# Performance work log

Measured on AMD Instinct MI355X. Metric: run time of the kernel, lower is better.

The kernel has to match this reference:

```python
import jax, jax.numpy as jnp
import numpy as np

B, N, DIM, HEADS = 8, 1024, 512, 8
HEAD_DIM = DIM // HEADS
SCALE = HEAD_DIM ** -0.5
NEG_BIG = -1.0e12


def setup_inputs() -> dict:
    key = jax.random.key(0)
    k_x, k_qw, k_qb, k_pw, k_pb = jax.random.split(key, 5)
    # torch nn.Linear layout: weight [out, in], y = x @ W.T + b
    s_qkv = (DIM) ** -0.5
    return {
        "x": jax.random.normal(k_x, (B, N, DIM), dtype=jnp.float32),
        "qkv_w": jax.random.uniform(k_qw, (3 * DIM, DIM), minval=-s_qkv, maxval=s_qkv, dtype=jnp.float32),
        "qkv_b": jax.random.uniform(k_qb, (3 * DIM,), minval=-s_qkv, maxval=s_qkv, dtype=jnp.float32),
        "proj_w": jax.random.uniform(k_pw, (DIM, DIM), minval=-s_qkv, maxval=s_qkv, dtype=jnp.float32),
        "proj_b": jax.random.uniform(k_pb, (DIM,), minval=-s_qkv, maxval=s_qkv, dtype=jnp.float32),
    }


def reference(x, qkv_w, qkv_b, proj_w, proj_b):
    b, n, c = x.shape
    qkv = x @ qkv_w.T + qkv_b                      # [B, N, 3*C]
    qkv = qkv.reshape(b, n, 3, HEADS, c // HEADS)
    qkv = jnp.transpose(qkv, (2, 0, 3, 1, 4))      # [3, B, H, N, hd]
    q, k, v = qkv[0], qkv[1], qkv[2]
    attn = jnp.einsum("bhqd,bhkd->bhqk", q, k) * SCALE  # [B, H, N, N]
    # bernoulli(p=0.5) mask added as -1e12 bias (deterministic key)
    mask = jax.random.bernoulli(jax.random.key(42), 0.5, attn.shape)
    attn = attn + mask.astype(attn.dtype) * NEG_BIG
    attn = jax.nn.softmax(attn, axis=-1)
    # dropout p=0.0 -> identity
    out = jnp.einsum("bhqk,bhkd->bhqd", attn, v)   # [B, H, N, hd]
    out = jnp.transpose(out, (0, 2, 1, 3)).reshape(b, n, c)
    return out @ proj_w.T + proj_b
```

## Files before the change

### kernel.cpp

```cpp
#include <hip/hip_runtime.h>
#include <stdint.h>

typedef uint32_t u32;
typedef unsigned long long u64;
using bf16x8 = __attribute__((ext_vector_type(8))) short;
using f32x4  = __attribute__((ext_vector_type(4))) float;

#define MFMA16(a, b, c) __builtin_amdgcn_mfma_f32_16x16x32_bf16((a), (b), (c), 0, 0, 0)

__device__ __forceinline__ unsigned short f2bf(float f) {
  u32 u = __builtin_bit_cast(u32, f);
  return (unsigned short)((u + 0x7FFFu + ((u >> 16) & 1u)) >> 16);
}

__device__ __forceinline__ void gl_lds16(const unsigned short* g, unsigned short* l) {
  __builtin_amdgcn_global_load_lds((const __attribute__((address_space(1))) void*)g,
                                   (__attribute__((address_space(3))) void*)l, 16, 0, 0);
}

__device__ __forceinline__ u32 rotl(u32 x, int r) {
  return __builtin_amdgcn_alignbit(x, x, 32 - r);
}
#define TFR(r) x0 += x1; x1 = rotl(x1, r) ^ x0;

__device__ __forceinline__ u32 tf_word(u32 j) {
  const u32 ks1 = 42u, ks2 = 0x1BD11BDAu ^ 42u;
  u32 x0 = 0u;
  u32 x1 = j + ks1;
  TFR(13) TFR(15) TFR(26) TFR(6)
  x0 += ks1; x1 += ks2 + 1u;
  TFR(17) TFR(29) TFR(16) TFR(24)
  x0 += ks2; x1 += 2u;
  TFR(13) TFR(15) TFR(26) TFR(6)
  x1 += ks1 + 3u;
  TFR(17) TFR(29) TFR(16) TFR(24)
  x0 += ks1; x1 += ks2 + 4u;
  TFR(13) TFR(15) TFR(26) TFR(6)
  x0 += ks2; x1 += 5u;
  return x0 ^ x1;
}

__global__ __launch_bounds__(256) void cvt_kernel(
    const float* __restrict__ x, const float* __restrict__ qw, const float* __restrict__ pw,
    unsigned short* __restrict__ xb, unsigned short* __restrict__ qwb,
    unsigned short* __restrict__ pwb) {
  int t = blockIdx.x * 256 + threadIdx.x;
  const float4* src; unsigned short* dst; int idx;
  if (t < 1048576)      { src = (const float4*)x;  dst = xb;  idx = t; }
  else if (t < 1245184) { src = (const float4*)qw; dst = qwb; idx = t - 1048576; }
  else                  { src = (const float4*)pw; dst = pwb; idx = t - 1245184; }
  float4 v = src[idx];
  ushort4 o = make_ushort4(f2bf(v.x), f2bf(v.y), f2bf(v.z), f2bf(v.w));
  ((ushort4*)dst)[idx] = o;
}

template<int EPI>
__global__ __launch_bounds__(256)
void gemm_kernel(const unsigned short* __restrict__ A, const unsigned short* __restrict__ Bm,
                 const float* __restrict__ bias, unsigned short* __restrict__ q_out,
                 unsigned short* __restrict__ k_out, unsigned short* __restrict__ vt_out,
                 float* __restrict__ f_out) {
  __shared__ __align__(16) unsigned short lA[128 * 32];
  __shared__ __align__(16) unsigned short lB[128 * 32];
  const int tid = threadIdx.x;
  const int lane = tid & 63, w = tid >> 6;
  const int hi = lane >> 4, lo = lane & 15;
  const int wm = w >> 1, wn = w & 1;
  const int m0 = blockIdx.y * 128, n0 = blockIdx.x * 128;
  const int srow = lane >> 2, skc = (lane & 3) * 8;

  f32x4 acc[4][4];
#pragma unroll
  for (int i = 0; i < 4; ++i)
#pragma unroll
    for (int j = 0; j < 4; ++j) acc[i][j] = (f32x4){0.f, 0.f, 0.f, 0.f};

  for (int kt = 0; kt < 16; ++kt) {
    const int k0 = kt * 32;
    __syncthreads();
#pragma unroll
    for (int c = 0; c < 2; ++c) {
      const int rr = (w * 2 + c) * 16 + srow;
      gl_lds16(A  + (size_t)(m0 + rr) * 512 + k0 + skc, &lA[(w * 2 + c) * 512]);
      gl_lds16(Bm + (size_t)(n0 + rr) * 512 + k0 + skc, &lB[(w * 2 + c) * 512]);
    }
    __syncthreads();

    bf16x8 af[4], bfr[4];
#pragma unroll
    for (int i = 0; i < 4; ++i) af[i]  = *(const bf16x8*)&lA[(wm * 64 + i * 16 + lo) * 32 + hi * 8];
#pragma unroll
    for (int i = 0; i < 4; ++i) bfr[i] = *(const bf16x8*)&lB[(wn * 64 + i * 16 + lo) * 32 + hi * 8];
#pragma unroll
    for (int i = 0; i < 4; ++i)
#pragma unroll
      for (int j = 0; j < 4; ++j)
        acc[i][j] = MFMA16(af[i], bfr[j], acc[i][j]);
  }

#pragma unroll
  for (int i = 0; i < 4; ++i) {
    const int rowb = m0 + wm * 64 + i * 16 + hi * 4;
#pragma unroll
    for (int j = 0; j < 4; ++j) {
      const int col = n0 + wn * 64 + j * 16 + lo;
      const float bv = bias[col];
      if (EPI == 0) {
        const int which = col >> 9, hh = (col >> 6) & 7, dd = col & 63;
        const float scl = (which == 0) ? 0.18033688011112042f : 1.0f;
#pragma unroll
        for (int r = 0; r < 4; ++r) {
          const int tok = rowb + r;
          const int b = tok >> 10, nt = tok & 1023;
          const int bh = b * 8 + hh;
          const unsigned short val = f2bf((acc[i][j][r] + bv) * scl);
          if (which == 0)      q_out[((size_t)((bh << 10) + nt)) * 64 + dd] = val;
          else if (which == 1) k_out[((size_t)((bh << 10) + nt)) * 64 + dd] = val;
          else                 vt_out[((size_t)bh * 64 + dd) * 1024 + nt] = val;
        }
      } else {
#pragma unroll
        for (int r = 0; r < 4; ++r)
          f_out[(size_t)(rowb + r) * 512 + col] = acc[i][j][r] + bv;
      }
    }
  }
}

__global__ __launch_bounds__(256, 8) void attn_kernel(
    const unsigned short* __restrict__ Qb, const unsigned short* __restrict__ Kb,
    const unsigned short* __restrict__ VTb, unsigned short* __restrict__ aout) {
  __shared__ __align__(16) unsigned short plds[4][1088];
  const int tid = threadIdx.x;
  const int lane = tid & 63, w = tid >> 6;
  const int hi = lane >> 4, lo = lane & 15;
  const int p = w & 1, half = w >> 1;
  const int bid = blockIdx.x;
  const int xcd = bid & 7, slot = bid >> 3;
  const int bh = (xcd << 3) | (slot >> 5);
  const int qg = slot & 31;
  const int qs = qg * 32 + p * 16;

  bf16x8 qf[2];
#pragma unroll
  for (int dh = 0; dh < 2; ++dh)
    qf[dh] = *(const bf16x8*)&Qb[((size_t)(bh << 10) + qs + lo) * 64 + dh * 32 + hi * 8];

  f32x4 acc[4];
  f32x4 sacc = (f32x4){0.f, 0.f, 0.f, 0.f};
#pragma unroll
  for (int dt = 0; dt < 4; ++dt) acc[dt] = (f32x4){0.f, 0.f, 0.f, 0.f};
  bf16x8 ones;
#pragma unroll
  for (int j = 0; j < 8; ++j) ones[j] = (short)0x3F80;

  const u32 jbase = ((u32)bh << 20) | ((u32)(qs + lo) << 10) | (u32)(hi * 4);
  const int ktbase = half * 8;
  unsigned short* mp = &plds[w][0];

  for (int i = 0; i < 8; ++i) {
    const int k0 = (ktbase + i) * 64;

#pragma unroll
    for (int t = 0; t < 4; ++t) {
      const unsigned short* kbp = &Kb[((size_t)(bh << 10) + k0 + t * 16 + lo) * 64 + hi * 8];
      f32x4 z = (f32x4){0.f, 0.f, 0.f, 0.f};
      z = MFMA16(*(const bf16x8*)kbp, qf[0], z);
      z = MFMA16(*(const bf16x8*)(kbp + 32), qf[1], z);

      float pv[4];
#pragma unroll
      for (int r = 0; r < 4; ++r) {
        const int keepn = (int)tf_word(jbase + (u32)(k0 + t * 16 + r));
        pv[r] = (keepn < 0) ? exp2f(z[r]) : 0.f;
      }
      u32 u0, u1;
      asm("v_cvt_pk_bf16_f32 %0, %1, %2" : "=v"(u0) : "v"(pv[0]), "v"(pv[1]));
      asm("v_cvt_pk_bf16_f32 %0, %1, %2" : "=v"(u1) : "v"(pv[2]), "v"(pv[3]));
      *reinterpret_cast<u64*>(&mp[lo * 68 + t * 16 + hi * 4]) = ((u64)u1 << 32) | (u64)u0;
    }

    bf16x8 pf[2];
#pragma unroll
    for (int ks = 0; ks < 2; ++ks)
      pf[ks] = *(const bf16x8*)&mp[lo * 68 + ks * 32 + hi * 8];
    sacc = MFMA16(pf[0], ones, sacc);
    sacc = MFMA16(pf[1], ones, sacc);
#pragma unroll
    for (int dt = 0; dt < 4; ++dt) {
      const unsigned short* vbp = &VTb[((size_t)(bh * 64 + dt * 16 + lo)) * 1024 + k0 + hi * 8];
      acc[dt] = MFMA16(pf[0], *(const bf16x8*)vbp, acc[dt]);
      acc[dt] = MFMA16(pf[1], *(const bf16x8*)(vbp + 32), acc[dt]);
    }
  }

  float* fb = ((float*)&plds[0][0]) + p * 1040;
  __syncthreads();
  if (half == 1) {
#pragma unroll
    for (int dt = 0; dt < 4; ++dt)
#pragma unroll
      for (int r = 0; r < 4; ++r)
        fb[(hi * 4 + r) * 64 + dt * 16 + lo] = acc[dt][r];
    if (lo == 0)
#pragma unroll
      for (int r = 0; r < 4; ++r) fb[1024 + hi * 4 + r] = sacc[r];
  }
  __syncthreads();
  if (half == 0) {
    const int b = bh >> 3, h = bh & 7;
#pragma unroll
    for (int r = 0; r < 4; ++r) {
      const float zt = sacc[r] + fb[1024 + hi * 4 + r];
      const float inv = 1.0f / zt;
      const int tok = (b << 10) + qs + hi * 4 + r;
#pragma unroll
      for (int dt = 0; dt < 4; ++dt) {
        const float av = acc[dt][r] + fb[(hi * 4 + r) * 64 + dt * 16 + lo];
        aout[(size_t)tok * 512 + h * 64 + dt * 16 + lo] = f2bf(av * inv);
      }
    }
  }
}

extern "C" void kernel_launch(void* const* d_in, const int* in_sizes, int n_in,
                              void* d_out, int out_size, void* d_ws, size_t ws_size,
                              hipStream_t stream) {
  const float* x      = (const float*)d_in[0];
  const float* qkv_w  = (const float*)d_in[1];
  const float* qkv_b  = (const float*)d_in[2];
  const float* proj_w = (const float*)d_in[3];
  const float* proj_b = (const float*)d_in[4];
  float* out = (float*)d_out;
  char* ws = (char*)d_ws;

  unsigned short* xb  = (unsigned short*)(ws);
  unsigned short* qwb = (unsigned short*)(ws +  8388608);
  unsigned short* pwb = (unsigned short*)(ws +  9961472);
  unsigned short* Qb  = (unsigned short*)(ws + 10485760);
  unsigned short* Kb  = (unsigned short*)(ws + 18874368);
  unsigned short* VTb = (unsigned short*)(ws + 27262976);

  cvt_kernel<<<5120, 256, 0, stream>>>(x, qkv_w, proj_w, xb, qwb, pwb);
  gemm_kernel<0><<<dim3(12, 64), 256, 0, stream>>>(xb, qwb, qkv_b, Qb, Kb, VTb, nullptr);
  attn_kernel<<<2048, 256, 0, stream>>>(Qb, Kb, VTb, xb);
  gemm_kernel<1><<<dim3(4, 64), 256, 0, stream>>>(xb, pwb, proj_b, nullptr, nullptr, nullptr, out);
}
```

Before: 205.7 us.

## Fuse fp32-to-bf16 conversion into GEMM loads and simplify mask/exp path

Removes the separate conversion kernel. The GEMMs now read fp32 x and fp32 weights directly, convert them in registers and store bf16 into LDS, in place of the async global-to-LDS loads. The attention mask now uses raw v_exp_f32 with a bitwise AND against the sign of the threefry word, replacing the branch around exp2f. This saves one launch and a write/read round trip of the bf16 copies, but weights are re-converted by every block and the GEMM loses direct-to-LDS loads, so more register traffic goes through the loop.

```diff
diff --git a/kernel.cpp b/kernel.cpp
--- a/kernel.cpp
+++ b/kernel.cpp
@@ -16,6 +16,12 @@
 __device__ __forceinline__ void gl_lds16(const unsigned short* g, unsigned short* l) {
   __builtin_amdgcn_global_load_lds((const __attribute__((address_space(1))) void*)g,
                                    (__attribute__((address_space(3))) void*)l, 16, 0, 0);
+}
+
+__device__ __forceinline__ u32 cvtpk(float a, float b) {
+  u32 r;
+  asm("v_cvt_pk_bf16_f32 %0, %1, %2" : "=v"(r) : "v"(a), "v"(b));
+  return r;
 }
 
 __device__ __forceinline__ u32 rotl(u32 x, int r) {
@@ -40,26 +46,11 @@
   return x0 ^ x1;
 }
 
-__global__ __launch_bounds__(256) void cvt_kernel(
-    const float* __restrict__ x, const float* __restrict__ qw, const float* __restrict__ pw,
-    unsigned short* __restrict__ xb, unsigned short* __restrict__ qwb,
-    unsigned short* __restrict__ pwb) {
-  int t = blockIdx.x * 256 + threadIdx.x;
-  const float4* src; unsigned short* dst; int idx;
-  if (t < 1048576)      { src = (const float4*)x;  dst = xb;  idx = t; }
-  else if (t < 1245184) { src = (const float4*)qw; dst = qwb; idx = t - 1048576; }
-  else                  { src = (const float4*)pw; dst = pwb; idx = t - 1245184; }
-  float4 v = src[idx];
-  ushort4 o = make_ushort4(f2bf(v.x), f2bf(v.y), f2bf(v.z), f2bf(v.w));
-  ((ushort4*)dst)[idx] = o;
-}
-
 template<int EPI>
 __global__ __launch_bounds__(256)
-void gemm_kernel(const unsigned short* __restrict__ A, const unsigned short* __restrict__ Bm,
-                 const float* __restrict__ bias, unsigned short* __restrict__ q_out,
-                 unsigned short* __restrict__ k_out, unsigned short* __restrict__ vt_out,
-                 float* __restrict__ f_out) {
+void gemm_kernel(const void* Ap, const float* B32, const float* __restrict__ bias,
+                 unsigned short* __restrict__ q_out, unsigned short* __restrict__ k_out,
+                 unsigned short* __restrict__ vt_out, float* __restrict__ f_out) {
   __shared__ __align__(16) unsigned short lA[128 * 32];
   __shared__ __align__(16) unsigned short lB[128 * 32];
   const int tid = threadIdx.x;
@@ -81,8 +72,20 @@
 #pragma unroll
     for (int c = 0; c < 2; ++c) {
       const int rr = (w * 2 + c) * 16 + srow;
-      gl_lds16(A  + (size_t)(m0 + rr) * 512 + k0 + skc, &lA[(w * 2 + c) * 512]);
-      gl_lds16(Bm + (size_t)(n0 + rr) * 512 + k0 + skc, &lB[(w * 2 + c) * 512]);
+      const int loff = (w * 2 + c) * 512 + srow * 32 + skc;
+      if (EPI == 0) {
+        const float* ga = (const float*)Ap + (size_t)(m0 + rr) * 512 + k0 + skc;
+        float4 a0 = *(const float4*)ga, a1 = *(const float4*)(ga + 4);
+        uint4 pa = {cvtpk(a0.x, a0.y), cvtpk(a0.z, a0.w), cvtpk(a1.x, a1.y), cvtpk(a1.z, a1.w)};
+        *reinterpret_cast<uint4*>(&lA[loff]) = pa;
+      } else {
+        gl_lds16((const unsigned short*)Ap + (size_t)(m0 + rr) * 512 + k0 + skc,
+                 &lA[(w * 2 + c) * 512]);
+      }
+      const float* gb = B32 + (size_t)(n0 + rr) * 512 + k0 + skc;
+      float4 b0 = *(const float4*)gb, b1 = *(const float4*)(gb + 4);
+      uint4 pb = {cvtpk(b0.x, b0.y), cvtpk(b0.z, b0.w), cvtpk(b1.x, b1.y), cvtpk(b1.z, b1.w)};
+      *reinterpret_cast<uint4*>(&lB[loff]) = pb;
     }
     __syncthreads();
 
@@ -171,12 +174,14 @@
       float pv[4];
 #pragma unroll
       for (int r = 0; r < 4; ++r) {
-        const int keepn = (int)tf_word(jbase + (u32)(k0 + t * 16 + r));
-        pv[r] = (keepn < 0) ? exp2f(z[r]) : 0.f;
-      }
-      u32 u0, u1;
-      asm("v_cvt_pk_bf16_f32 %0, %1, %2" : "=v"(u0) : "v"(pv[0]), "v"(pv[1]));
-      asm("v_cvt_pk_bf16_f32 %0, %1, %2" : "=v"(u1) : "v"(pv[2]), "v"(pv[3]));
+        const u32 tf = tf_word(jbase + (u32)(k0 + t * 16 + r));
+        float e;
+        asm("v_exp_f32 %0, %1" : "=v"(e) : "v"(z[r]));
+        const u32 eb = __builtin_bit_cast(u32, e) & (u32)((int)tf >> 31);
+        pv[r] = __builtin_bit_cast(float, eb);
+      }
+      const u32 u0 = cvtpk(pv[0], pv[1]);
+      const u32 u1 = cvtpk(pv[2], pv[3]);
       *reinterpret_cast<u64*>(&mp[lo * 68 + t * 16 + hi * 4]) = ((u64)u1 << 32) | (u64)u0;
     }
 
@@ -234,15 +239,12 @@
   float* out = (float*)d_out;
   char* ws = (char*)d_ws;
 
-  unsigned short* xb  = (unsigned short*)(ws);
-  unsigned short* qwb = (unsigned short*)(ws +  8388608);
-  unsigned short* pwb = (unsigned short*)(ws +  9961472);
-  unsigned short* Qb  = (unsigned short*)(ws + 10485760);
-  unsigned short* Kb  = (unsigned short*)(ws + 18874368);
-  unsigned short* VTb = (unsigned short*)(ws + 27262976);
-
-  cvt_kernel<<<5120, 256, 0, stream>>>(x, qkv_w, proj_w, xb, qwb, pwb);
-  gemm_kernel<0><<<dim3(12, 64), 256, 0, stream>>>(xb, qwb, qkv_b, Qb, Kb, VTb, nullptr);
-  attn_kernel<<<2048, 256, 0, stream>>>(Qb, Kb, VTb, xb);
-  gemm_kernel<1><<<dim3(4, 64), 256, 0, stream>>>(xb, pwb, proj_b, nullptr, nullptr, nullptr, out);
-}
+  unsigned short* Qb  = (unsigned short*)(ws);
+  unsigned short* Kb  = (unsigned short*)(ws +  8388608);
+  unsigned short* VTb = (unsigned short*)(ws + 16777216);
+  unsigned short* ao  = (unsigned short*)(ws + 25165824);
+
+  gemm_kernel<0><<<dim3(12, 64), 256, 0, stream>>>(x, qkv_w, qkv_b, Qb, Kb, VTb, nullptr);
+  attn_kernel<<<2048, 256, 0, stream>>>(Qb, Kb, VTb, ao);
+  gemm_kernel<1><<<dim3(4, 64), 256, 0, stream>>>(ao, proj_w, proj_b, nullptr, nullptr, nullptr, out);
+}
```

After: 218.9 us. +6.4%, slower.
